# Kernel optimization log

Measured on AMD Instinct MI355X. Metric: run time of the kernel, lower is better.

Reference implementation:

```python
import jax, jax.numpy as jnp
import numpy as np

D_MODEL = 2048
N_HEADS = 16
D_K = D_MODEL // N_HEADS
BATCH = 4
SEQ = 2048


def setup_inputs() -> dict:
    key = jax.random.key(0)
    ks = jax.random.split(key, 9)
    s = 1.0 / np.sqrt(D_MODEL)
    return {
        "x": jax.random.normal(ks[0], (BATCH, SEQ, D_MODEL), dtype=jnp.float32),
        "wq_w": jax.random.normal(ks[1], (D_MODEL, D_MODEL), dtype=jnp.float32) * s,
        "wq_b": jax.random.normal(ks[2], (D_MODEL,), dtype=jnp.float32) * 0.02,
        "wk_w": jax.random.normal(ks[3], (D_MODEL, D_MODEL), dtype=jnp.float32) * s,
        "wk_b": jax.random.normal(ks[4], (D_MODEL,), dtype=jnp.float32) * 0.02,
        "wv_w": jax.random.normal(ks[5], (D_MODEL, D_MODEL), dtype=jnp.float32) * s,
        "wv_b": jax.random.normal(ks[6], (D_MODEL,), dtype=jnp.float32) * 0.02,
        "wo_w": jax.random.normal(ks[7], (D_MODEL, D_MODEL), dtype=jnp.float32) * s,
        "wo_b": jax.random.normal(ks[8], (D_MODEL,), dtype=jnp.float32) * 0.02,
    }


def reference(x, wq_w, wq_b, wk_w, wk_b, wv_w, wv_b, wo_w, wo_b):
    b, s, _ = x.shape
    # Linear projections (torch Linear: x @ W^T + b)
    def split_heads(t):  # (b, s, d_model) -> (b, h, s, d_k)
        return t.reshape(b, s, N_HEADS, D_K).transpose(0, 2, 1, 3)
    q = split_heads(x @ wq_w.T + wq_b)
    k = split_heads(x @ wk_w.T + wk_b)
    v = split_heads(x @ wv_w.T + wv_b)
    scale = 1.0 / jnp.sqrt(jnp.asarray(D_K, dtype=x.dtype))
    scores = jnp.einsum("bhqd,bhkd->bhqk", q, k) * scale  # (b, h, s, s)
    attn = jax.nn.softmax(scores, axis=-1)
    ctx = jnp.einsum("bhqk,bhkd->bhqd", attn, v)
    ctx = ctx.transpose(0, 2, 1, 3).reshape(b, s, D_MODEL)
    out = ctx @ wo_w.T + wo_b
    return out
```

## Files before the change

kernel.cpp:

```cpp
#include <hip/hip_runtime.h>
#include <hip/hip_bf16.h>
#include <math.h>

typedef __attribute__((ext_vector_type(8))) short short8;
typedef __attribute__((ext_vector_type(4))) float f32x4;
typedef __attribute__((ext_vector_type(16))) float f32x16;
typedef __attribute__((ext_vector_type(4))) unsigned short u16x4;
typedef __attribute__((ext_vector_type(8))) unsigned short u16x8;
typedef __attribute__((ext_vector_type(4))) unsigned int u32x4;
typedef __attribute__((ext_vector_type(2))) int i32x2;
typedef unsigned short u16;
typedef unsigned int u32;

#define DM 2048
#define SQ 2048
#define NB 4
#define NH 16
#define DKH 128
#define KT 64
#define NT (SQ / KT)
#define LD3 (3 * DM)
#define QSCALE (0.08838834764831845f * 1.4426950408889634f)

__device__ __forceinline__ u16 f2bf(float f) {
  unsigned u = __float_as_uint(f);
  u += 0x7fffu + ((u >> 16) & 1u);
  return (u16)(u >> 16);
}

__device__ __forceinline__ u32 cvtpk(float lo, float hi) {
  u32 r;
  asm("v_cvt_pk_bf16_f32 %0, %1, %2" : "=v"(r) : "v"(lo), "v"(hi));
  return r;
}

__device__ __forceinline__ void gload16(const u16* g, u16* lds) {
  __builtin_amdgcn_global_load_lds(
      (const __attribute__((address_space(1))) unsigned int*)g,
      (__attribute__((address_space(3))) unsigned int*)lds, 16, 0, 0);
}

__device__ __forceinline__ int paddr16(int r, int k, int nkt) {
  const int cid = (((r >> 8) * nkt + (k >> 6)) << 5) | (((r >> 7) & 1) << 4) |
                  (((r >> 5) & 3) << 2) | ((k >> 4) & 3);
  return (cid << 9) + (((r & 31) | (((k >> 3) & 1) << 3 << 2)) << 3) + (k & 7);
}

__device__ __forceinline__ void pinv(int idx, int nkt, int& r, int& k) {
  const int e8 = idx & 63;
  const int cid = idx >> 6;
  const int kt = (cid >> 5) % nkt;
  const int rt = (cid >> 5) / nkt;
  r = (rt << 8) + (((cid >> 4) & 1) << 7) + (((cid >> 2) & 3) << 5) + (e8 & 31);
  k = (kt << 6) + ((cid & 3) << 4) + ((e8 >> 5) << 3);
}

__global__ void cvt_x_p(const float* __restrict__ in, u16* __restrict__ out) {
  const int idx = blockIdx.x * 256 + threadIdx.x;
  int r, k;
  pinv(idx, 32, r, k);
  const float4 v0 = *(const float4*)(in + (size_t)r * DM + k);
  const float4 v1 = *(const float4*)(in + (size_t)r * DM + k + 4);
  u16x8 o;
  o[0] = f2bf(v0.x); o[1] = f2bf(v0.y); o[2] = f2bf(v0.z); o[3] = f2bf(v0.w);
  o[4] = f2bf(v1.x); o[5] = f2bf(v1.y); o[6] = f2bf(v1.z); o[7] = f2bf(v1.w);
  *(u16x8*)(out + (size_t)idx * 8) = o;
}

__global__ void cvt_w_p(const float* __restrict__ w0, const float* __restrict__ w1,
                        const float* __restrict__ w2, const float* __restrict__ w3,
                        u16* __restrict__ dq, u16* __restrict__ dw) {
  const int sel = blockIdx.y;
  const float* src;
  switch (sel) {
    case 0: src = w0; break;
    case 1: src = w1; break;
    case 2: src = w2; break;
    default: src = w3; break;
  }
  const int idx = blockIdx.x * 256 + threadIdx.x;
  int r, k;
  pinv(idx, 32, r, k);
  const float4 v0 = *(const float4*)(src + (size_t)r * DM + k);
  const float4 v1 = *(const float4*)(src + (size_t)r * DM + k + 4);
  u16x8 o;
  o[0] = f2bf(v0.x); o[1] = f2bf(v0.y); o[2] = f2bf(v0.z); o[3] = f2bf(v0.w);
  o[4] = f2bf(v1.x); o[5] = f2bf(v1.y); o[6] = f2bf(v1.z); o[7] = f2bf(v1.w);
  u16* dst = (sel < 3) ? (dq + (size_t)sel * DM * DM) : dw;
  *(u16x8*)(dst + (size_t)idx * 8) = o;
}


#define STG_A(T, HALF)                                                       \
  do {                                                                       \
    _Pragma("unroll") for (int uu = 0; uu < 2; ++uu) {                       \
      const int j_ = w * 2 + uu;                                             \
      gload16(As + ((((T) * 32 + (HALF) * 16 + j_) << 9) + l * 8),           \
              &smA[((T) & 1) * 16384 + ((HALF) * 16 + j_) * 512]);           \
    }                                                                        \
  } while (0)

#define STG_B(T, HALF)                                                       \
  do {                                                                       \
    _Pragma("unroll") for (int uu = 0; uu < 2; ++uu) {                       \
      const int j_ = w * 2 + uu;                                             \
      gload16(Bs + ((((T) * 32 + (HALF) * 16 + j_) << 9) + l * 8),           \
              &smB[((T) & 1) * 16384 + ((HALF) * 16 + j_) * 512]);           \
    }                                                                        \
  } while (0)

#define LDA(QM)                                                            \
  do {                                                                     \
    const int rb_ = wr * 4 + (QM) * 2;                                     \
    const u16* p_ = &smA[bi * 16384 + rb_ * 2048 + l * 8];                 \
    _Pragma("unroll") for (int s = 0; s < 4; ++s) {                        \
      af[0][s] = *(const short8*)&p_[s * 512];                             \
      af[1][s] = *(const short8*)&p_[2048 + s * 512];                      \
    }                                                                      \
  } while (0)

#define LDB(QN)                                                            \
  do {                                                                     \
    const int rb_ = wc * 2 + (QN);                                         \
    const u16* p_ = &smB[bi * 16384 + rb_ * 2048 + l * 8];                 \
    _Pragma("unroll") for (int s = 0; s < 4; ++s)                          \
      bf[QN][s] = *(const short8*)&p_[s * 512];                            \
  } while (0)

#define MFMA_Q(QM, QN)                                                             \
  __builtin_amdgcn_s_setprio(1);                                                   \
  _Pragma("unroll") for (int s = 0; s < 4; ++s) {                                  \
    acc[(QM) * 2][(QN)] = __builtin_amdgcn_mfma_f32_32x32x16_bf16(                 \
        af[0][s], bf[QN][s], acc[(QM) * 2][(QN)], 0, 0, 0);                        \
    acc[(QM) * 2 + 1][(QN)] = __builtin_amdgcn_mfma_f32_32x32x16_bf16(             \
        af[1][s], bf[QN][s], acc[(QM) * 2 + 1][(QN)], 0, 0, 0);                    \
  }                                                                                \
  __builtin_amdgcn_s_setprio(0);

template <int MODE>
__global__ __launch_bounds__(512, 2) void gemm8p(
    const u16* __restrict__ A, const u16* __restrict__ B,
    const float* __restrict__ bq, const float* __restrict__ bk,
    const float* __restrict__ bvp, void* __restrict__ Cout,
    int M, int N, int K) {
  __shared__ u16 smA[2 * 16384];
  __shared__ u16 smB[2 * 16384];
  const int tid = threadIdx.x;
  const int w = tid >> 6, l = tid & 63;
  const int c5 = l & 31, hi = l >> 5;
  const int wr = w >> 2, wc = w & 3;

  int flat = blockIdx.x + (int)gridDim.x * (int)blockIdx.y;
  const int nwg = (int)(gridDim.x * gridDim.y);
  flat = (flat & 7) * (nwg >> 3) + (flat >> 3);
  const int m0 = (flat / (int)gridDim.x) * 256, n0 = (flat % (int)gridDim.x) * 256;

  const int NSTEP = K / 64;
  f32x16 acc[4][2] = {};

  const u16* As = A + (size_t)(m0 >> 8) * NSTEP * 16384;
  const u16* Bs = B + (size_t)(n0 >> 8) * NSTEP * 16384;

  STG_A(0, 0); STG_A(0, 1); STG_B(0, 0); STG_B(0, 1);
  STG_B(1, 0); STG_A(1, 0);
  asm volatile("s_waitcnt vmcnt(4)" ::: "memory");
  __builtin_amdgcn_s_barrier();

  short8 af[2][4], bf[2][4];
  for (int t = 0; t < NSTEP; ++t) {
    const int bi = t & 1;
    LDA(0); LDB(0);
    if (t + 1 < NSTEP) STG_B(t + 1, 1);
    MFMA_Q(0, 0);
    __builtin_amdgcn_s_barrier();
    LDB(1);
    if (t + 1 < NSTEP) STG_A(t + 1, 1);
    MFMA_Q(0, 1);
    __builtin_amdgcn_s_barrier();
    LDA(1);
    if (t + 2 < NSTEP) STG_B(t + 2, 0);
    MFMA_Q(1, 1);
    __builtin_amdgcn_s_barrier();
    if (t + 2 < NSTEP) STG_A(t + 2, 0);
    MFMA_Q(1, 0);
    if (t + 2 < NSTEP)
      asm volatile("s_waitcnt vmcnt(4)" ::: "memory");
    else if (t + 1 < NSTEP)
      asm volatile("s_waitcnt vmcnt(0)" ::: "memory");
    __builtin_amdgcn_s_barrier();
  }

#pragma unroll
  for (int nf = 0; nf < 2; ++nf) {
    const int col = n0 + wc * 64 + nf * 32 + c5;
    float bval, os;
    if (MODE == 0) {
      const int seg = col >> 11;
      const float* bp = seg == 0 ? bq : (seg == 1 ? bk : bvp);
      bval = bp[col & (DM - 1)];
      os = (seg == 0) ? QSCALE : 1.0f;
    } else {
      bval = bq[col];
      os = 1.0f;
    }
#pragma unroll
    for (int mf = 0; mf < 4; ++mf) {
#pragma unroll
      for (int r = 0; r < 16; ++r) {
        const int row = m0 + wr * 128 + mf * 32 + (r & 3) + 8 * (r >> 2) + 4 * hi;
        const float v = (acc[mf][nf][r] + bval) * os;
        if (MODE == 1)
          ((float*)Cout)[(size_t)row * N + col] = v;
        else
          ((u16*)Cout)[(size_t)row * N + col] = f2bf(v);
      }
    }
  }
}

__global__ __launch_bounds__(512, 2) void attn(
    const u16* __restrict__ QKV, u16* __restrict__ O) {
  __shared__ u16 smK[2 * 8192];
  __shared__ u16 smV[9216];
  __shared__ float alScr[8 * 32];

  const u16* Qp = QKV;
  const u16* Kp = QKV + DM;
  const u16* Vp = QKV + 2 * DM;

  const int tid = threadIdx.x;
  const int w = tid >> 6, l = tid & 63;
  const int c5 = l & 31, hi = l >> 5;

  int flat = blockIdx.x + ((int)blockIdx.y << 3) + ((int)blockIdx.z << 7);
  flat = (flat & 7) * 64 + (flat >> 3);
  const int qt = flat & 7, h = (flat >> 3) & 15, b = flat >> 7;

  const int q0 = qt * 256 + w * 32;
  const size_t rowb = (size_t)b * SQ;
  const int hoff = h * DKH;

  short8 qf[8];
#pragma unroll
  for (int ds = 0; ds < 8; ++ds)
    qf[ds] = *(const short8*)&Qp[(rowb + q0 + c5) * LD3 + hoff + ds * 16 + hi * 8];

  f32x16 o[4] = {};
  float mrow = -1e30f, lsum = 0.f;

  const int vdg = tid >> 5;
  const int kvp = (tid & 31) * 2;
  u16x8 va, vb;

  {
#pragma unroll
    for (int uu = 0; uu < 2; ++uu) {
      const int u = w * 2 + uu;
      const int row = u * 4 + (l >> 4);
      const int col16 = (l & 15) ^ (row & 15);
      gload16(&Kp[(rowb + row) * LD3 + hoff + col16 * 8], &smK[u * 512]);
    }
    const u16* vp = &Vp[(rowb + kvp) * LD3 + hoff + vdg * 8];
    va = *(const u16x8*)vp;
    vb = *(const u16x8*)(vp + LD3);
#pragma unroll
    for (int i = 0; i < 8; ++i) {
      const int d = vdg * 8 + i;
      *(u32*)&smV[d * 72 + kvp] = (u32)va[i] | ((u32)vb[i] << 16);
    }
  }
  __syncthreads();

  int buf = 0;
  for (int t = 0; t < NT; ++t) {
    const int nb = buf ^ 1;
    if (t + 1 < NT) {
      const size_t kvr = rowb + (size_t)(t + 1) * KT;
#pragma unroll
      for (int uu = 0; uu < 2; ++uu) {
        const int u = w * 2 + uu;
        const int row = u * 4 + (l >> 4);
        const int col16 = (l & 15) ^ (row & 15);
        gload16(&Kp[(kvr + row) * LD3 + hoff + col16 * 8], &smK[nb * 8192 + u * 512]);
      }
      const u16* vp = &Vp[(kvr + kvp) * LD3 + hoff + vdg * 8];
      va = *(const u16x8*)vp;
      vb = *(const u16x8*)(vp + LD3);
    }

    f32x16 s[2] = {};
    __builtin_amdgcn_s_setprio(1);
#pragma unroll
    for (int ds = 0; ds < 8; ++ds) {
#pragma unroll
      for (int ni = 0; ni < 2; ++ni) {
        const int row = ni * 32 + c5;
        const short8 kf = *(const short8*)&smK[buf * 8192 + row * 128 + (((ds << 1) | hi) ^ (row & 15)) * 8];
        s[ni] = __builtin_amdgcn_mfma_f32_32x32x16_bf16(kf, qf[ds], s[ni], 0, 0, 0);
      }
    }
    __builtin_amdgcn_s_setprio(0);

    float mt[16];
#pragma unroll
    for (int i = 0; i < 16; ++i) mt[i] = fmaxf(s[0][i], s[1][i]);
#pragma unroll
    for (int st = 8; st >= 1; st >>= 1)
#pragma unroll
      for (int i = 0; i < st; ++i) mt[i] = fmaxf(mt[i], mt[i + st]);
    i32x2 sw = __builtin_amdgcn_permlane32_swap(__float_as_int(mt[0]), __float_as_int(mt[0]), false, false);
    const float gmax = fmaxf(__int_as_float(sw.x), __int_as_float(sw.y));

    if (__any(gmax > mrow + 10.0f)) {
      const float mn = fmaxf(mrow, gmax);
      const float al = exp2f(mrow - mn);
      mrow = mn;
      lsum *= al;
      alScr[w * 32 + c5] = al;
#pragma unroll
      for (int r = 0; r < 16; ++r) {
        const float av = alScr[w * 32 + (r & 3) + 8 * (r >> 2) + 4 * hi];
#pragma unroll
        for (int dg = 0; dg < 4; ++dg) o[dg][r] *= av;
      }
    }

    float ps0 = 0.f, ps1 = 0.f;
#pragma unroll
    for (int i = 0; i < 16; ++i) {
      const float p0 = exp2f(s[0][i] - mrow);
      const float p1 = exp2f(s[1][i] - mrow);
      s[0][i] = p0; s[1][i] = p1;
      ps0 += p0; ps1 += p1;
    }
    lsum += ps0 + ps1;

    __builtin_amdgcn_s_setprio(1);
#pragma unroll
    for (int ks = 0; ks < 4; ++ks) {
      const int b0 = (ks & 1) * 8;
      const int ni = ks >> 1;
      const u32 A0 = cvtpk(s[ni][b0 + 0], s[ni][b0 + 1]);
      const u32 A1 = cvtpk(s[ni][b0 + 4], s[ni][b0 + 5]);
      const u32 B0 = cvtpk(s[ni][b0 + 2], s[ni][b0 + 3]);
      const u32 B1 = cvtpk(s[ni][b0 + 6], s[ni][b0 + 7]);
      const i32x2 r0 = __builtin_amdgcn_permlane32_swap((int)A0, (int)A1, false, false);
      const i32x2 r1 = __builtin_amdgcn_permlane32_swap((int)B0, (int)B1, false, false);
      u32x4 paw;
      paw.x = (u32)r0.x; paw.y = (u32)r1.x; paw.z = (u32)r0.y; paw.w = (u32)r1.y;
      const short8 pa = *(const short8*)&paw;
#pragma unroll
      for (int dg = 0; dg < 4; ++dg) {
        const int rowd = dg * 32 + c5;
        const short8 vf = *(const short8*)&smV[rowd * 72 + ks * 16 + hi * 8];
        o[dg] = __builtin_amdgcn_mfma_f32_32x32x16_bf16(pa, vf, o[dg], 0, 0, 0);
      }
    }
    __builtin_amdgcn_s_setprio(0);

    __syncthreads();
    if (t + 1 < NT) {
#pragma unroll
      for (int i = 0; i < 8; ++i) {
        const int d = vdg * 8 + i;
        *(u32*)&smV[d * 72 + kvp] = (u32)va[i] | ((u32)vb[i] << 16);
      }
      __syncthreads();
    }
    buf = nb;
  }

  {
    const i32x2 sl = __builtin_amdgcn_permlane32_swap(__float_as_int(lsum), __float_as_int(lsum), false, false);
    const float tot = __int_as_float(sl.x) + __int_as_float(sl.y);
    alScr[w * 32 + c5] = 1.0f / tot;
  }
#pragma unroll
  for (int r = 0; r < 16; ++r) {
    const int qloc = (r & 3) + 8 * (r >> 2) + 4 * hi;
    const float inv = alScr[w * 32 + qloc];
    const int rowg = (int)rowb + q0 + qloc;
#pragma unroll
    for (int dg = 0; dg < 4; ++dg)
      O[paddr16(rowg, hoff + dg * 32 + c5, 32)] = f2bf(o[dg][r] * inv);
  }
}

extern "C" void kernel_launch(void* const* d_in, const int* in_sizes, int n_in,
                              void* d_out, int out_size, void* d_ws, size_t ws_size,
                              hipStream_t stream) {
  const float* x    = (const float*)d_in[0];
  const float* wq_w = (const float*)d_in[1];
  const float* wq_b = (const float*)d_in[2];
  const float* wk_w = (const float*)d_in[3];
  const float* wk_b = (const float*)d_in[4];
  const float* wv_w = (const float*)d_in[5];
  const float* wv_b = (const float*)d_in[6];
  const float* wo_w = (const float*)d_in[7];
  const float* wo_b = (const float*)d_in[8];
  float* out = (float*)d_out;

  u16* p = (u16*)d_ws;
  u16* xb  = p; p += (size_t)NB * SQ * DM;
  u16* wqb = p; p += (size_t)3 * DM * DM;
  u16* wob = p; p += (size_t)DM * DM;
  u16* QKV = p; p += (size_t)NB * SQ * 3 * DM;
  u16* ctx = xb;

  cvt_x_p<<<dim3(NB * SQ * DM / 2048), dim3(256), 0, stream>>>(x, xb);
  cvt_w_p<<<dim3(DM * DM / 2048, 4), dim3(256), 0, stream>>>(wq_w, wk_w, wv_w, wo_w, wqb, wob);

  dim3 gg3(3 * DM / 256, (NB * SQ) / 256);
  gemm8p<0><<<gg3, dim3(512), 0, stream>>>(xb, wqb, wq_b, wk_b, wv_b, QKV,
                                           NB * SQ, 3 * DM, DM);

  attn<<<dim3(SQ / 256, NH, NB), dim3(512), 0, stream>>>(QKV, ctx);

  dim3 ggo(DM / 256, (NB * SQ) / 256);
  gemm8p<1><<<ggo, dim3(512), 0, stream>>>(ctx, wob, wo_b, nullptr, nullptr, out,
                                           NB * SQ, DM, DM);
}
```

Measured before the change: 544.6 us.

## Software-pipeline LDS fragment loads across quadrants in projection GEMM

Restructures the GEMM main loop so each quadrant's LDS fragment loads are issued one quadrant ahead of their MFMAs, with separate A/B register sets. The next tile's first fragments are prefetched in the last quadrant of the current tile, and vmcnt waits are spread across sub-steps. The loop is peeled for the last two tiles. This aims to hide LDS latency behind MFMA work, at the cost of more live registers under the 512-thread, 2-blocks-per-CU launch bound.

```diff
diff --git a/kernel.cpp b/kernel.cpp
--- a/kernel.cpp
+++ b/kernel.cpp
@@ -91,6 +91,11 @@
 }
 
 
+#define VM6 asm volatile("s_waitcnt vmcnt(6)" ::: "memory")
+#define VM4 asm volatile("s_waitcnt vmcnt(4)" ::: "memory")
+#define VM0 asm volatile("s_waitcnt vmcnt(0)" ::: "memory")
+#define VMN ((void)0)
+
 #define STG_A(T, HALF)                                                       \
   do {                                                                       \
     _Pragma("unroll") for (int uu = 0; uu < 2; ++uu) {                       \
@@ -109,33 +114,59 @@
     }                                                                        \
   } while (0)
 
-#define LDA(QM)                                                            \
+#define LD_A(DST, QM, BI)                                                  \
   do {                                                                     \
-    const int rb_ = wr * 4 + (QM) * 2;                                     \
-    const u16* p_ = &smA[bi * 16384 + rb_ * 2048 + l * 8];                 \
+    const u16* p_ = &smA[(BI)*16384 + (wr * 4 + (QM) * 2) * 2048 + l * 8]; \
     _Pragma("unroll") for (int s = 0; s < 4; ++s) {                        \
-      af[0][s] = *(const short8*)&p_[s * 512];                             \
-      af[1][s] = *(const short8*)&p_[2048 + s * 512];                      \
+      DST[0][s] = *(const short8*)&p_[s * 512];                            \
+      DST[1][s] = *(const short8*)&p_[2048 + s * 512];                     \
     }                                                                      \
   } while (0)
 
-#define LDB(QN)                                                            \
+#define LD_B(DST, QN, BI)                                                  \
   do {                                                                     \
-    const int rb_ = wc * 2 + (QN);                                         \
-    const u16* p_ = &smB[bi * 16384 + rb_ * 2048 + l * 8];                 \
+    const u16* p_ = &smB[(BI)*16384 + (wc * 2 + (QN)) * 2048 + l * 8];     \
     _Pragma("unroll") for (int s = 0; s < 4; ++s)                          \
-      bf[QN][s] = *(const short8*)&p_[s * 512];                            \
+      DST[s] = *(const short8*)&p_[s * 512];                               \
   } while (0)
 
-#define MFMA_Q(QM, QN)                                                             \
+#define MFQ(QM, QN, AA, BB)                                                        \
   __builtin_amdgcn_s_setprio(1);                                                   \
   _Pragma("unroll") for (int s = 0; s < 4; ++s) {                                  \
     acc[(QM) * 2][(QN)] = __builtin_amdgcn_mfma_f32_32x32x16_bf16(                 \
-        af[0][s], bf[QN][s], acc[(QM) * 2][(QN)], 0, 0, 0);                        \
+        AA[0][s], BB[s], acc[(QM) * 2][(QN)], 0, 0, 0);                            \
     acc[(QM) * 2 + 1][(QN)] = __builtin_amdgcn_mfma_f32_32x32x16_bf16(             \
-        af[1][s], bf[QN][s], acc[(QM) * 2 + 1][(QN)], 0, 0, 0);                    \
+        AA[1][s], BB[s], acc[(QM) * 2 + 1][(QN)], 0, 0, 0);                        \
   }                                                                                \
   __builtin_amdgcn_s_setprio(0);
+
+#define GTILE(T, S01, S23, R23, VM1_, VM2_, VM3_)                          \
+  do {                                                                     \
+    const int bi = (T) & 1, bn = ((T) + 1) & 1;                            \
+                                      \
+    if (S01) STG_B((T) + 1, 1);                                            \
+    LD_A(a1, 1, bi);                                                       \
+    MFQ(0, 0, a0, b0);                                                     \
+    __builtin_amdgcn_s_barrier();                                          \
+                                      \
+    if (S01) STG_A((T) + 1, 1);                                            \
+    LD_B(b1, 1, bi);                                                       \
+    MFQ(1, 0, a1, b0);                                                     \
+    VM1_;                                                                  \
+    __builtin_amdgcn_s_barrier();                                          \
+                                    \
+    if (S23) STG_B((T) + 2, 0);                                            \
+    if (R23) LD_B(b0, 0, bn);                                              \
+    MFQ(0, 1, a0, b1);                                                     \
+    VM2_;                                                                  \
+    __builtin_amdgcn_s_barrier();                                          \
+                                    \
+    if (S23) STG_A((T) + 2, 0);                                            \
+    if (R23) LD_A(a0, 0, bn);                                              \
+    MFQ(1, 1, a1, b1);                                                     \
+    VM3_;                                                                  \
+    __builtin_amdgcn_s_barrier();                                          \
+  } while (0)
 
 template <int MODE>
 __global__ __launch_bounds__(512, 2) void gemm8p(
@@ -161,34 +192,19 @@
   const u16* As = A + (size_t)(m0 >> 8) * NSTEP * 16384;
   const u16* Bs = B + (size_t)(n0 >> 8) * NSTEP * 16384;
 
-  STG_A(0, 0); STG_A(0, 1); STG_B(0, 0); STG_B(0, 1);
+  STG_B(0, 0); STG_A(0, 0); STG_B(0, 1); STG_A(0, 1);
   STG_B(1, 0); STG_A(1, 0);
-  asm volatile("s_waitcnt vmcnt(4)" ::: "memory");
+  VM0;
   __builtin_amdgcn_s_barrier();
 
-  short8 af[2][4], bf[2][4];
-  for (int t = 0; t < NSTEP; ++t) {
-    const int bi = t & 1;
-    LDA(0); LDB(0);
-    if (t + 1 < NSTEP) STG_B(t + 1, 1);
-    MFMA_Q(0, 0);
-    __builtin_amdgcn_s_barrier();
-    LDB(1);
-    if (t + 1 < NSTEP) STG_A(t + 1, 1);
-    MFMA_Q(0, 1);
-    __builtin_amdgcn_s_barrier();
-    LDA(1);
-    if (t + 2 < NSTEP) STG_B(t + 2, 0);
-    MFMA_Q(1, 1);
-    __builtin_amdgcn_s_barrier();
-    if (t + 2 < NSTEP) STG_A(t + 2, 0);
-    MFMA_Q(1, 0);
-    if (t + 2 < NSTEP)
-      asm volatile("s_waitcnt vmcnt(4)" ::: "memory");
-    else if (t + 1 < NSTEP)
-      asm volatile("s_waitcnt vmcnt(0)" ::: "memory");
-    __builtin_amdgcn_s_barrier();
-  }
+  short8 a0[2][4], a1[2][4], b0[4], b1[4];
+  LD_A(a0, 0, 0);
+  LD_B(b0, 0, 0);
+
+  for (int t = 0; t < NSTEP - 2; ++t)
+    GTILE(t, 1, 1, 1, VM6, VM6, VM4);
+  GTILE(NSTEP - 2, 1, 0, 1, VM6, VM4, VM0);
+  GTILE(NSTEP - 1, 0, 0, 0, VMN, VMN, VMN);
 
 #pragma unroll
   for (int nf = 0; nf < 2; ++nf) {
@@ -338,12 +354,12 @@
     __builtin_amdgcn_s_setprio(1);
 #pragma unroll
     for (int ks = 0; ks < 4; ++ks) {
-      const int b0 = (ks & 1) * 8;
+      const int b0_ = (ks & 1) * 8;
       const int ni = ks >> 1;
-      const u32 A0 = cvtpk(s[ni][b0 + 0], s[ni][b0 + 1]);
-      const u32 A1 = cvtpk(s[ni][b0 + 4], s[ni][b0 + 5]);
-      const u32 B0 = cvtpk(s[ni][b0 + 2], s[ni][b0 + 3]);
-      const u32 B1 = cvtpk(s[ni][b0 + 6], s[ni][b0 + 7]);
+      const u32 A0 = cvtpk(s[ni][b0_ + 0], s[ni][b0_ + 1]);
+      const u32 A1 = cvtpk(s[ni][b0_ + 4], s[ni][b0_ + 5]);
+      const u32 B0 = cvtpk(s[ni][b0_ + 2], s[ni][b0_ + 3]);
+      const u32 B1 = cvtpk(s[ni][b0_ + 6], s[ni][b0_ + 7]);
       const i32x2 r0 = __builtin_amdgcn_permlane32_swap((int)A0, (int)A1, false, false);
       const i32x2 r1 = __builtin_amdgcn_permlane32_swap((int)B0, (int)B1, false, false);
       u32x4 paw;
```

New measurement: 580.6 us. 1.07x slower.

## Load K fragments directly from global and double-buffer V in LDS

Applied to the files above, without the earlier changes.

The attention kernel stops staging K tiles through shared memory. Each lane now reads its K MFMA fragments straight from global memory (relying on L1/L2), while V gets a double-buffered LDS tile, so the loop needs one barrier per iteration instead of two. This removes LDS traffic and a barrier for K, at the cost of many uncoalesced, latency-exposed global loads placed directly before the QK MFMAs, each wave fetching the full K tile independently.

```diff
diff --git a/kernel.cpp b/kernel.cpp
--- a/kernel.cpp
+++ b/kernel.cpp
@@ -220,8 +220,7 @@
 
 __global__ __launch_bounds__(512, 2) void attn(
     const u16* __restrict__ QKV, u16* __restrict__ O) {
-  __shared__ u16 smK[2 * 8192];
-  __shared__ u16 smV[9216];
+  __shared__ u16 smV[2 * 9216];
   __shared__ float alScr[8 * 32];
 
   const u16* Qp = QKV;
@@ -252,14 +251,10 @@
   const int kvp = (tid & 31) * 2;
   u16x8 va, vb;
 
+  const u16* k0 = &Kp[(rowb + c5) * LD3 + hoff + hi * 8];
+  const u16* k1 = k0 + (size_t)32 * LD3;
+
   {
-#pragma unroll
-    for (int uu = 0; uu < 2; ++uu) {
-      const int u = w * 2 + uu;
-      const int row = u * 4 + (l >> 4);
-      const int col16 = (l & 15) ^ (row & 15);
-      gload16(&Kp[(rowb + row) * LD3 + hoff + col16 * 8], &smK[u * 512]);
-    }
     const u16* vp = &Vp[(rowb + kvp) * LD3 + hoff + vdg * 8];
     va = *(const u16x8*)vp;
     vb = *(const u16x8*)(vp + LD3);
@@ -273,17 +268,8 @@
 
   int buf = 0;
   for (int t = 0; t < NT; ++t) {
-    const int nb = buf ^ 1;
     if (t + 1 < NT) {
-      const size_t kvr = rowb + (size_t)(t + 1) * KT;
-#pragma unroll
-      for (int uu = 0; uu < 2; ++uu) {
-        const int u = w * 2 + uu;
-        const int row = u * 4 + (l >> 4);
-        const int col16 = (l & 15) ^ (row & 15);
-        gload16(&Kp[(kvr + row) * LD3 + hoff + col16 * 8], &smK[nb * 8192 + u * 512]);
-      }
-      const u16* vp = &Vp[(kvr + kvp) * LD3 + hoff + vdg * 8];
+      const u16* vp = &Vp[(rowb + (size_t)(t + 1) * KT + kvp) * LD3 + hoff + vdg * 8];
       va = *(const u16x8*)vp;
       vb = *(const u16x8*)(vp + LD3);
     }
@@ -292,14 +278,14 @@
     __builtin_amdgcn_s_setprio(1);
 #pragma unroll
     for (int ds = 0; ds < 8; ++ds) {
-#pragma unroll
-      for (int ni = 0; ni < 2; ++ni) {
-        const int row = ni * 32 + c5;
-        const short8 kf = *(const short8*)&smK[buf * 8192 + row * 128 + (((ds << 1) | hi) ^ (row & 15)) * 8];
-        s[ni] = __builtin_amdgcn_mfma_f32_32x32x16_bf16(kf, qf[ds], s[ni], 0, 0, 0);
-      }
+      const short8 kf0 = *(const short8*)(k0 + ds * 16);
+      const short8 kf1 = *(const short8*)(k1 + ds * 16);
+      s[0] = __builtin_amdgcn_mfma_f32_32x32x16_bf16(kf0, qf[ds], s[0], 0, 0, 0);
+      s[1] = __builtin_amdgcn_mfma_f32_32x32x16_bf16(kf1, qf[ds], s[1], 0, 0, 0);
     }
     __builtin_amdgcn_s_setprio(0);
+    k0 += (size_t)KT * LD3;
+    k1 += (size_t)KT * LD3;
 
     float mt[16];
 #pragma unroll
@@ -338,12 +324,12 @@
     __builtin_amdgcn_s_setprio(1);
 #pragma unroll
     for (int ks = 0; ks < 4; ++ks) {
-      const int b0 = (ks & 1) * 8;
+      const int b0_ = (ks & 1) * 8;
       const int ni = ks >> 1;
-      const u32 A0 = cvtpk(s[ni][b0 + 0], s[ni][b0 + 1]);
-      const u32 A1 = cvtpk(s[ni][b0 + 4], s[ni][b0 + 5]);
-      const u32 B0 = cvtpk(s[ni][b0 + 2], s[ni][b0 + 3]);
-      const u32 B1 = cvtpk(s[ni][b0 + 6], s[ni][b0 + 7]);
+      const u32 A0 = cvtpk(s[ni][b0_ + 0], s[ni][b0_ + 1]);
+      const u32 A1 = cvtpk(s[ni][b0_ + 4], s[ni][b0_ + 5]);
+      const u32 B0 = cvtpk(s[ni][b0_ + 2], s[ni][b0_ + 3]);
+      const u32 B1 = cvtpk(s[ni][b0_ + 6], s[ni][b0_ + 7]);
       const i32x2 r0 = __builtin_amdgcn_permlane32_swap((int)A0, (int)A1, false, false);
       const i32x2 r1 = __builtin_amdgcn_permlane32_swap((int)B0, (int)B1, false, false);
       u32x4 paw;
@@ -352,22 +338,22 @@
 #pragma unroll
       for (int dg = 0; dg < 4; ++dg) {
         const int rowd = dg * 32 + c5;
-        const short8 vf = *(const short8*)&smV[rowd * 72 + ks * 16 + hi * 8];
+        const short8 vf = *(const short8*)&smV[buf * 9216 + rowd * 72 + ks * 16 + hi * 8];
         o[dg] = __builtin_amdgcn_mfma_f32_32x32x16_bf16(pa, vf, o[dg], 0, 0, 0);
       }
     }
     __builtin_amdgcn_s_setprio(0);
 
-    __syncthreads();
     if (t + 1 < NT) {
+      const int nb = buf ^ 1;
 #pragma unroll
       for (int i = 0; i < 8; ++i) {
         const int d = vdg * 8 + i;
-        *(u32*)&smV[d * 72 + kvp] = (u32)va[i] | ((u32)vb[i] << 16);
+        *(u32*)&smV[nb * 9216 + d * 72 + kvp] = (u32)va[i] | ((u32)vb[i] << 16);
       }
-      __syncthreads();
-    }
-    buf = nb;
+    }
+    __syncthreads();
+    buf ^= 1;
   }
 
   {
```

Result: slower. 722.6 us (+32.7%).

## Write V transposed from QKV GEMM epilogue and async-load it in attention

Applied to the files above, without the earlier changes.

The QKV projection epilogue now writes Q and K into a 2*DM-wide buffer and writes V transposed (head-dim major, row contiguous) into a separate buffer. The attention kernel then loads V tiles with direct global-to-LDS loads into a double-buffered swizzled LDS tile, the same way it loads K. This removes the per-tile register transpose, the extra LDS stores and the second barrier per iteration. In exchange the GEMM epilogue does strided transposed stores for the V third, and the attention kernel uses more LDS.

```diff
diff --git a/kernel.cpp b/kernel.cpp
--- a/kernel.cpp
+++ b/kernel.cpp
@@ -19,7 +19,8 @@
 #define DKH 128
 #define KT 64
 #define NT (SQ / KT)
-#define LD3 (3 * DM)
+#define LD2 (2 * DM)
+#define NROW (NB * SQ)
 #define QSCALE (0.08838834764831845f * 1.4426950408889634f)
 
 __device__ __forceinline__ u16 f2bf(float f) {
@@ -142,7 +143,7 @@
     const u16* __restrict__ A, const u16* __restrict__ B,
     const float* __restrict__ bq, const float* __restrict__ bk,
     const float* __restrict__ bvp, void* __restrict__ Cout,
-    int M, int N, int K) {
+    void* __restrict__ Cout2, int M, int N, int K) {
   __shared__ u16 smA[2 * 16384];
   __shared__ u16 smB[2 * 16384];
   const int tid = threadIdx.x;
@@ -193,40 +194,55 @@
 #pragma unroll
   for (int nf = 0; nf < 2; ++nf) {
     const int col = n0 + wc * 64 + nf * 32 + c5;
-    float bval, os;
     if (MODE == 0) {
       const int seg = col >> 11;
       const float* bp = seg == 0 ? bq : (seg == 1 ? bk : bvp);
-      bval = bp[col & (DM - 1)];
-      os = (seg == 0) ? QSCALE : 1.0f;
+      const float bval = bp[col & (DM - 1)];
+      const float os = (seg == 0) ? QSCALE : 1.0f;
+      if (seg < 2) {
+#pragma unroll
+        for (int mf = 0; mf < 4; ++mf)
+#pragma unroll
+          for (int r = 0; r < 16; ++r) {
+            const int row = m0 + wr * 128 + mf * 32 + (r & 3) + 8 * (r >> 2) + 4 * hi;
+            ((u16*)Cout)[(size_t)row * LD2 + col] = f2bf((acc[mf][nf][r] + bval) * os);
+          }
+      } else {
+        u16* vbase = (u16*)Cout2 + (size_t)(col - 2 * DM) * NROW;
+#pragma unroll
+        for (int mf = 0; mf < 4; ++mf) {
+          const int row0 = m0 + wr * 128 + mf * 32 + 4 * hi;
+#pragma unroll
+          for (int g2 = 0; g2 < 4; ++g2) {
+            u16x4 pk;
+#pragma unroll
+            for (int j = 0; j < 4; ++j)
+              pk[j] = f2bf(acc[mf][nf][g2 * 4 + j] + bval);
+            *(u16x4*)(vbase + row0 + 8 * g2) = pk;
+          }
+        }
+      }
     } else {
-      bval = bq[col];
-      os = 1.0f;
-    }
-#pragma unroll
-    for (int mf = 0; mf < 4; ++mf) {
-#pragma unroll
-      for (int r = 0; r < 16; ++r) {
-        const int row = m0 + wr * 128 + mf * 32 + (r & 3) + 8 * (r >> 2) + 4 * hi;
-        const float v = (acc[mf][nf][r] + bval) * os;
-        if (MODE == 1)
-          ((float*)Cout)[(size_t)row * N + col] = v;
-        else
-          ((u16*)Cout)[(size_t)row * N + col] = f2bf(v);
-      }
+      const float bval = bq[col];
+#pragma unroll
+      for (int mf = 0; mf < 4; ++mf)
+#pragma unroll
+        for (int r = 0; r < 16; ++r) {
+          const int row = m0 + wr * 128 + mf * 32 + (r & 3) + 8 * (r >> 2) + 4 * hi;
+          ((float*)Cout)[(size_t)row * N + col] = acc[mf][nf][r] + bval;
+        }
     }
   }
 }
 
 __global__ __launch_bounds__(512, 2) void attn(
-    const u16* __restrict__ QKV, u16* __restrict__ O) {
+    const u16* __restrict__ QK, const u16* __restrict__ VT, u16* __restrict__ O) {
   __shared__ u16 smK[2 * 8192];
-  __shared__ u16 smV[9216];
+  __shared__ u16 smV[2 * 8192];
   __shared__ float alScr[8 * 32];
 
-  const u16* Qp = QKV;
-  const u16* Kp = QKV + DM;
-  const u16* Vp = QKV + 2 * DM;
+  const u16* Qp = QK;
+  const u16* Kp = QK + DM;
 
   const int tid = threadIdx.x;
   const int w = tid >> 6, l = tid & 63;
@@ -243,14 +259,12 @@
   short8 qf[8];
 #pragma unroll
   for (int ds = 0; ds < 8; ++ds)
-    qf[ds] = *(const short8*)&Qp[(rowb + q0 + c5) * LD3 + hoff + ds * 16 + hi * 8];
+    qf[ds] = *(const short8*)&Qp[(rowb + q0 + c5) * LD2 + hoff + ds * 16 + hi * 8];
 
   f32x16 o[4] = {};
   float mrow = -1e30f, lsum = 0.f;
 
-  const int vdg = tid >> 5;
-  const int kvp = (tid & 31) * 2;
-  u16x8 va, vb;
+  const u16* vsrc = VT + (size_t)(hoff + (l >> 3)) * NROW + rowb + ((l & 7) ^ (l >> 3)) * 8;
 
   {
 #pragma unroll
@@ -258,15 +272,8 @@
       const int u = w * 2 + uu;
       const int row = u * 4 + (l >> 4);
       const int col16 = (l & 15) ^ (row & 15);
-      gload16(&Kp[(rowb + row) * LD3 + hoff + col16 * 8], &smK[u * 512]);
-    }
-    const u16* vp = &Vp[(rowb + kvp) * LD3 + hoff + vdg * 8];
-    va = *(const u16x8*)vp;
-    vb = *(const u16x8*)(vp + LD3);
-#pragma unroll
-    for (int i = 0; i < 8; ++i) {
-      const int d = vdg * 8 + i;
-      *(u32*)&smV[d * 72 + kvp] = (u32)va[i] | ((u32)vb[i] << 16);
+      gload16(&Kp[(rowb + row) * LD2 + hoff + col16 * 8], &smK[u * 512]);
+      gload16(vsrc + (size_t)u * 8 * NROW, &smV[u * 512]);
     }
   }
   __syncthreads();
@@ -276,16 +283,15 @@
     const int nb = buf ^ 1;
     if (t + 1 < NT) {
       const size_t kvr = rowb + (size_t)(t + 1) * KT;
+      const int kv1 = (t + 1) * KT;
 #pragma unroll
       for (int uu = 0; uu < 2; ++uu) {
         const int u = w * 2 + uu;
         const int row = u * 4 + (l >> 4);
         const int col16 = (l & 15) ^ (row & 15);
-        gload16(&Kp[(kvr + row) * LD3 + hoff + col16 * 8], &smK[nb * 8192 + u * 512]);
+        gload16(&Kp[(kvr + row) * LD2 + hoff + col16 * 8], &smK[nb * 8192 + u * 512]);
+        gload16(vsrc + (size_t)u * 8 * NROW + kv1, &smV[nb * 8192 + u * 512]);
       }
-      const u16* vp = &Vp[(kvr + kvp) * LD3 + hoff + vdg * 8];
-      va = *(const u16x8*)vp;
-      vb = *(const u16x8*)(vp + LD3);
     }
 
     f32x16 s[2] = {};
@@ -338,12 +344,12 @@
     __builtin_amdgcn_s_setprio(1);
 #pragma unroll
     for (int ks = 0; ks < 4; ++ks) {
-      const int b0 = (ks & 1) * 8;
+      const int b0_ = (ks & 1) * 8;
       const int ni = ks >> 1;
-      const u32 A0 = cvtpk(s[ni][b0 + 0], s[ni][b0 + 1]);
-      const u32 A1 = cvtpk(s[ni][b0 + 4], s[ni][b0 + 5]);
-      const u32 B0 = cvtpk(s[ni][b0 + 2], s[ni][b0 + 3]);
-      const u32 B1 = cvtpk(s[ni][b0 + 6], s[ni][b0 + 7]);
+      const u32 A0 = cvtpk(s[ni][b0_ + 0], s[ni][b0_ + 1]);
+      const u32 A1 = cvtpk(s[ni][b0_ + 4], s[ni][b0_ + 5]);
+      const u32 B0 = cvtpk(s[ni][b0_ + 2], s[ni][b0_ + 3]);
+      const u32 B1 = cvtpk(s[ni][b0_ + 6], s[ni][b0_ + 7]);
       const i32x2 r0 = __builtin_amdgcn_permlane32_swap((int)A0, (int)A1, false, false);
       const i32x2 r1 = __builtin_amdgcn_permlane32_swap((int)B0, (int)B1, false, false);
       u32x4 paw;
@@ -352,21 +358,13 @@
 #pragma unroll
       for (int dg = 0; dg < 4; ++dg) {
         const int rowd = dg * 32 + c5;
-        const short8 vf = *(const short8*)&smV[rowd * 72 + ks * 16 + hi * 8];
+        const short8 vf = *(const short8*)&smV[buf * 8192 + rowd * 64 + (((ks * 2 + hi) ^ (c5 & 7))) * 8];
         o[dg] = __builtin_amdgcn_mfma_f32_32x32x16_bf16(pa, vf, o[dg], 0, 0, 0);
       }
     }
     __builtin_amdgcn_s_setprio(0);
 
     __syncthreads();
-    if (t + 1 < NT) {
-#pragma unroll
-      for (int i = 0; i < 8; ++i) {
-        const int d = vdg * 8 + i;
-        *(u32*)&smV[d * 72 + kvp] = (u32)va[i] | ((u32)vb[i] << 16);
-      }
-      __syncthreads();
-    }
     buf = nb;
   }
 
@@ -401,22 +399,23 @@
   float* out = (float*)d_out;
 
   u16* p = (u16*)d_ws;
-  u16* xb  = p; p += (size_t)NB * SQ * DM;
+  u16* xb  = p; p += (size_t)NROW * DM;
   u16* wqb = p; p += (size_t)3 * DM * DM;
   u16* wob = p; p += (size_t)DM * DM;
-  u16* QKV = p; p += (size_t)NB * SQ * 3 * DM;
+  u16* QKb = p; p += (size_t)NROW * LD2;
+  u16* VTb = p; p += (size_t)DM * NROW;
   u16* ctx = xb;
 
-  cvt_x_p<<<dim3(NB * SQ * DM / 2048), dim3(256), 0, stream>>>(x, xb);
+  cvt_x_p<<<dim3(NROW * DM / 2048), dim3(256), 0, stream>>>(x, xb);
   cvt_w_p<<<dim3(DM * DM / 2048, 4), dim3(256), 0, stream>>>(wq_w, wk_w, wv_w, wo_w, wqb, wob);
 
-  dim3 gg3(3 * DM / 256, (NB * SQ) / 256);
-  gemm8p<0><<<gg3, dim3(512), 0, stream>>>(xb, wqb, wq_b, wk_b, wv_b, QKV,
-                                           NB * SQ, 3 * DM, DM);
-
-  attn<<<dim3(SQ / 256, NH, NB), dim3(512), 0, stream>>>(QKV, ctx);
-
-  dim3 ggo(DM / 256, (NB * SQ) / 256);
+  dim3 gg3(3 * DM / 256, NROW / 256);
+  gemm8p<0><<<gg3, dim3(512), 0, stream>>>(xb, wqb, wq_b, wk_b, wv_b, QKb, VTb,
+                                           NROW, 3 * DM, DM);
+
+  attn<<<dim3(SQ / 256, NH, NB), dim3(512), 0, stream>>>(QKb, VTb, ctx);
+
+  dim3 ggo(DM / 256, NROW / 256);
   gemm8p<1><<<ggo, dim3(512), 0, stream>>>(ctx, wob, wo_b, nullptr, nullptr, out,
-                                           NB * SQ, DM, DM);
-}
+                                           nullptr, NROW, DM, DM);
+}
```

Measured after the change: 549.6 us. About the same (+0.9%).
